# Performance work log

Measured on AMD Instinct MI355X. Metric: run time of the kernel, lower is better.

The kernel has to match this reference:

```python
import jax, jax.numpy as jnp
import numpy as np

B, S, DM, H, FF = 2, 2048, 1024, 16, 4096
DH = DM // H
EPS = 1e-5


def setup_inputs() -> dict:
    key = jax.random.key(0)
    ks = jax.random.split(key, 16)
    s = 0.02
    return {
        "x": jax.random.normal(ks[0], (B, S, DM), jnp.float32),
        "mask": jnp.ones((B, S), jnp.int32),
        "Wq": jax.random.normal(ks[1], (DM, DM), jnp.float32) * s,
        "bq": jnp.zeros((DM,), jnp.float32),
        "Wk": jax.random.normal(ks[2], (DM, DM), jnp.float32) * s,
        "bk": jnp.zeros((DM,), jnp.float32),
        "Wv": jax.random.normal(ks[3], (DM, DM), jnp.float32) * s,
        "bv": jnp.zeros((DM,), jnp.float32),
        "Wo": jax.random.normal(ks[4], (DM, DM), jnp.float32) * s,
        "bo": jnp.zeros((DM,), jnp.float32),
        "W1": jax.random.normal(ks[5], (DM, FF), jnp.float32) * s,
        "b1": jnp.zeros((FF,), jnp.float32),
        "W2": jax.random.normal(ks[6], (FF, DM), jnp.float32) * s,
        "b2": jnp.zeros((DM,), jnp.float32),
        "g1": jnp.ones((DM,), jnp.float32),
        "beta1": jnp.zeros((DM,), jnp.float32),
        "g2": jnp.ones((DM,), jnp.float32),
        "beta2": jnp.zeros((DM,), jnp.float32),
    }


def _layer_norm(x, g, b):
    mu = jnp.mean(x, axis=-1, keepdims=True)
    var = jnp.var(x, axis=-1, keepdims=True)
    return (x - mu) * jax.lax.rsqrt(var + EPS) * g + b


def reference(x, mask, Wq, bq, Wk, bk, Wv, bv, Wo, bo, W1, b1, W2, b2, g1, beta1, g2, beta2):
    # --- hollow multi-head attention ---
    q = (x @ Wq + bq).reshape(B, S, H, DH)
    k = (x @ Wk + bk).reshape(B, S, H, DH)
    v = (x @ Wv + bv).reshape(B, S, H, DH)
    scores = jnp.einsum("bqhd,bkhd->bhqk", q, k) / jnp.sqrt(jnp.float32(DH))
    # triu(diag=1) and tril(diag=-1) masks kill everything off-diagonal
    diag = jnp.eye(S, dtype=bool)  # [S, S]
    scores = jnp.where(diag[None, None], scores, -jnp.inf)
    attn = jax.nn.softmax(scores, axis=-1)
    out = jnp.einsum("bhqk,bkhd->bqhd", attn, v).reshape(B, S, DM)
    attn_out = out @ Wo + bo
    # --- residual + LN1 ---
    h = _layer_norm(x + attn_out, g1, beta1)
    # --- FFN ---
    ff = jax.nn.relu(h @ W1 + b1) @ W2 + b2
    # --- residual + LN2 ---
    return _layer_norm(h + ff, g2, beta2)
```

## Files before the change

### kernel.cpp

```cpp
#include <hip/hip_runtime.h>
#include <stdint.h>

typedef __bf16 bf16x8 __attribute__((ext_vector_type(8)));
typedef float f32x4 __attribute__((ext_vector_type(4)));

__device__ __forceinline__ uint16_t f2bf(float f) {
  union { float f; uint32_t u; } c; c.f = f;
  uint32_t u = c.u;
  u += 0x7fffu + ((u >> 16) & 1u);
  return (uint16_t)(u >> 16);
}
__device__ __forceinline__ float bf2f(uint16_t u) {
  union { uint32_t u; float f; } c; c.u = (uint32_t)u << 16; return c.f;
}

__device__ __forceinline__ void cvt_body(const float* __restrict__ in,
                                         uint16_t* __restrict__ out, int i) {
  float4 v = reinterpret_cast<const float4*>(in)[i];
  ushort4 o;
  o.x = f2bf(v.x); o.y = f2bf(v.y); o.z = f2bf(v.z); o.w = f2bf(v.w);
  reinterpret_cast<ushort4*>(out)[i] = o;
}

__global__ void prep_kernel(const float* __restrict__ x, const float* __restrict__ Wv,
                            const float* __restrict__ Wo, const float* __restrict__ W1,
                            const float* __restrict__ W2, const float* __restrict__ bv,
                            const float* __restrict__ bo,
                            uint16_t* __restrict__ xb, uint16_t* __restrict__ wvb,
                            uint16_t* __restrict__ woT, uint16_t* __restrict__ w1t,
                            uint16_t* __restrict__ w2t, float* __restrict__ bc) {
  __shared__ float tsh[32][33];
  __shared__ float red[8][32];
  int b = blockIdx.x;
  const int t = threadIdx.x;
  if (b < 4096) { cvt_body(x, xb, b * 256 + t); return; }
  b -= 4096;
  if (b < 1024) { cvt_body(Wv, wvb, b * 256 + t); return; }
  b -= 1024;

  const float* tin = nullptr; uint16_t* tout = nullptr;
  int R = 0, C = 0, bx = 0, by = 0;
  if (b < 1024) {
    tin = Wo; tout = woT; R = 1024; C = 1024; bx = b & 31; by = b >> 5;
  } else if (b < 1024 + 4096) {
    const int bb = b - 1024;
    tin = W1; tout = w1t; R = 1024; C = 4096; bx = bb & 127; by = bb >> 7;
  } else if (b < 1024 + 8192) {
    const int bb = b - (1024 + 4096);
    tin = W2; tout = w2t; R = 4096; C = 1024; bx = bb & 31; by = bb >> 5;
  } else {
    const int jb = b - (1024 + 8192);
    const int jl = t & 31, kg = t >> 5;
    const int j = jb * 32 + jl;
    float s = 0.f;
    const int k0 = kg * 128;
    for (int k = k0; k < k0 + 128; ++k) s += bv[k] * Wo[(size_t)k * 1024 + j];
    red[kg][jl] = s;
    __syncthreads();
    if (kg == 0) {
      float acc = bo[j];
#pragma unroll
      for (int q = 0; q < 8; ++q) acc += red[q][jl];
      bc[j] = acc;
    }
    return;
  }
  const int tx = t & 31, ty = t >> 5;
  const int c0 = bx * 32, r0 = by * 32;
#pragma unroll
  for (int i = 0; i < 4; ++i)
    tsh[ty + i * 8][tx] = tin[(size_t)(r0 + ty + i * 8) * C + (c0 + tx)];
  __syncthreads();
#pragma unroll
  for (int i = 0; i < 4; ++i)
    tout[(size_t)(c0 + ty + i * 8) * R + (r0 + tx)] = f2bf(tsh[tx][ty + i * 8]);
}

constexpr int BM = 128, BN = 128, BK = 64;

template <int MODE>
__launch_bounds__(256, 2)
__global__ void gemm2ph_kernel(const uint16_t* __restrict__ A, const uint16_t* __restrict__ Bt,
                               const float* __restrict__ bias, const float* __restrict__ res,
                               void* __restrict__ out, int M, int N, int Klen, int lda, int ldb) {
  __shared__ uint16_t sAB[2][2][BM * BK];
  const int tid  = threadIdx.x;
  const int lane = tid & 63;
  const int wave = tid >> 6;

  const int nwg = gridDim.x * gridDim.y;
  int wg = blockIdx.y * gridDim.x + blockIdx.x;
  wg = (wg & 7) * (nwg >> 3) + (wg >> 3);
  const int bx = wg % gridDim.x, by = wg / gridDim.x;
  const int m0 = by * BM, n0 = bx * BN;

  const int z = blockIdx.z;
  A  += (size_t)z * Klen;
  Bt += (size_t)z * Klen;

  const int wm = (wave >> 1) * 64;
  const int wn = (wave & 1) * 64;

  f32x4 acc[4][4] = {};

  const int srow = tid >> 3;
  const int scol = ((tid & 7) ^ (srow & 7)) * 8;
  const uint16_t* ga[4];
  const uint16_t* gb[4];
  uint32_t loff[4];
#pragma unroll
  for (int g = 0; g < 4; ++g) {
    const int row = srow + 32 * g;
    ga[g] = A + (size_t)(m0 + row) * lda + scol;
    gb[g] = Bt + (size_t)(n0 + row) * ldb + scol;
    loff[g] = (uint32_t)(tid + g * 256) * 8;
  }

  const int fr = lane & 15;
  const int hi = lane >> 4;
  const int rx = fr & 7;

  const int nk = Klen / BK;

#define STAGE2(buf, kt)                                                                   \
  {                                                                                       \
    _Pragma("unroll")                                                                     \
    for (int g = 0; g < 4; ++g) {                                                         \
      __builtin_amdgcn_global_load_lds(                                                   \
          (const __attribute__((address_space(1))) uint32_t*)(ga[g] + (size_t)(kt) * BK), \
          (__attribute__((address_space(3))) uint32_t*)(&sAB[buf][0][loff[g]]), 16, 0, 0);\
      __builtin_amdgcn_global_load_lds(                                                   \
          (const __attribute__((address_space(1))) uint32_t*)(gb[g] + (size_t)(kt) * BK), \
          (__attribute__((address_space(3))) uint32_t*)(&sAB[buf][1][loff[g]]), 16, 0, 0);\
    }                                                                                     \
  }

  STAGE2(0, 0);
  __syncthreads();

  int cur = 0;
  for (int kt = 0; kt < nk; ++kt) {
    if (kt + 1 < nk) STAGE2(cur ^ 1, kt + 1);
    const uint16_t* pA = &sAB[cur][0][0];
    const uint16_t* pB = &sAB[cur][1][0];
    bf16x8 af[4][2], bb[4][2];
#pragma unroll
    for (int m = 0; m < 4; ++m)
#pragma unroll
      for (int ks = 0; ks < 2; ++ks) {
        const int slot = (ks * 4 + hi) ^ rx;
        af[m][ks] = *reinterpret_cast<const bf16x8*>(pA + (wm + m * 16 + fr) * BK + slot * 8);
        bb[m][ks] = *reinterpret_cast<const bf16x8*>(pB + (wn + m * 16 + fr) * BK + slot * 8);
      }
#pragma unroll
    for (int ks = 0; ks < 2; ++ks)
#pragma unroll
      for (int m = 0; m < 4; ++m)
#pragma unroll
        for (int n = 0; n < 4; ++n)
          acc[m][n] = __builtin_amdgcn_mfma_f32_16x16x32_bf16(af[m][ks], bb[n][ks], acc[m][n], 0, 0, 0);
    __syncthreads();
    cur ^= 1;
  }
#undef STAGE2

  const int cn  = lane & 15;
  const int cm4 = (lane >> 4) * 4;
  uint16_t* outp = (uint16_t*)out + (size_t)z * M * N;
#pragma unroll
  for (int m = 0; m < 4; ++m) {
#pragma unroll
    for (int n = 0; n < 4; ++n) {
      const int gm = m0 + wm + m * 16 + cm4;
      const int gn = n0 + wn + n * 16 + cn;
      const float bbv = bias ? bias[gn] : 0.f;
#pragma unroll
      for (int r = 0; r < 4; ++r) {
        const size_t idx = (size_t)(gm + r) * N + gn;
        const float vv = acc[m][n][r] + bbv;
        if constexpr (MODE == 0) {
          outp[idx] = f2bf(vv);
        } else {
          ((uint16_t*)out)[idx] = f2bf(vv + res[idx]);
        }
      }
    }
  }
}

__global__ void comb4_kernel(const uint16_t* __restrict__ wp, size_t stride,
                             uint16_t* __restrict__ o, int n4) {
  const int i = blockIdx.x * 256 + threadIdx.x;
  if (i >= n4) return;
  float4 v = {0.f, 0.f, 0.f, 0.f};
#pragma unroll
  for (int zz = 0; zz < 4; ++zz) {
    const ushort4 p = reinterpret_cast<const ushort4*>(wp + zz * stride)[i];
    v.x += bf2f(p.x); v.y += bf2f(p.y); v.z += bf2f(p.z); v.w += bf2f(p.w);
  }
  ushort4 r;
  r.x = f2bf(v.x); r.y = f2bf(v.y); r.z = f2bf(v.z); r.w = f2bf(v.w);
  reinterpret_cast<ushort4*>(o)[i] = r;
}

template <int MODE>
__launch_bounds__(512, 2)
__global__ void gemm8ph_kernel(const uint16_t* __restrict__ A, const uint16_t* __restrict__ Bt,
                               const float* __restrict__ bias, void* __restrict__ out,
                               int M, int N, int Klen, int lda, int ldb) {
  extern __shared__ uint16_t lds[];
  const int tid  = threadIdx.x;
  const int lane = tid & 63;
  const int wave = tid >> 6;

  const int nwg = gridDim.x * gridDim.y;
  int wg = blockIdx.y * gridDim.x + blockIdx.x;
  wg = (wg & 7) * (nwg >> 3) + (wg >> 3);
  const int bx = wg % gridDim.x, by = wg / gridDim.x;
  const int m0 = by * 256, n0 = bx * 256;

  const int z = blockIdx.z;
  A  += (size_t)z * Klen;
  Bt += (size_t)z * Klen;

  const int wm = (wave >> 2) * 128;
  const int wn = (wave & 3) * 64;

  f32x4 acc[8][4] = {};

  const int srw = tid >> 3;
  const int sp  = tid & 7;
  const uint16_t* gu[8];
#pragma unroll
  for (int u = 0; u < 8; ++u) {
    const uint16_t* base = (u < 4) ? A + (size_t)(m0 + u * 64) * lda
                                   : Bt + (size_t)(n0 + (u - 4) * 64) * ldb;
    const int ld = (u < 4) ? lda : ldb;
    gu[u] = base + (size_t)srw * ld + ((sp ^ (srw & 7)) * 8);
  }

  const int nk = Klen / 64;

#define STAGE8(T, U)                                                                          \
  if ((T) < nk) {                                                                             \
    __builtin_amdgcn_global_load_lds(                                                         \
        (const __attribute__((address_space(1))) uint32_t*)(gu[U] + (size_t)(T) * 64),        \
        (__attribute__((address_space(3))) uint32_t*)(lds + ((T) & 1) * 32768 + (U) * 4096 +  \
                                                      tid * 8),                               \
        16, 0, 0);                                                                            \
  }

  const int fr = lane & 15;
  const int hi = lane >> 4;
  int aoff[8];
#pragma unroll
  for (int m = 0; m < 8; ++m) {
    const int u = (wm >> 6) + (m >> 2);
    const int R = (m & 3) * 16 + fr;
    aoff[m] = u * 4096 + R * 64 + ((hi ^ (R & 7)) * 8);
  }
  int boff[4];
#pragma unroll
  for (int n = 0; n < 4; ++n) {
    const int u = 4 + (wn >> 6);
    const int R = n * 16 + fr;
    boff[n] = u * 4096 + R * 64 + ((hi ^ (R & 7)) * 8);
  }

  STAGE8(0, 0); STAGE8(0, 1); STAGE8(0, 2); STAGE8(0, 3);
  STAGE8(0, 4); STAGE8(0, 5); STAGE8(0, 6); STAGE8(0, 7);
  STAGE8(1, 4); STAGE8(1, 5); STAGE8(1, 6); STAGE8(1, 7);
  asm volatile("s_waitcnt vmcnt(4)" ::: "memory");
  __builtin_amdgcn_s_barrier();

#define LD8(off) (*reinterpret_cast<const bf16x8*>(bufp + (off)))
#define PHASE_MFMA32(KS)                                                      \
  __builtin_amdgcn_s_setprio(1);                                              \
  _Pragma("unroll") for (int mm = 0; mm < 8; ++mm)                            \
    _Pragma("unroll") for (int n = 0; n < 4; ++n)                             \
      acc[mm][n] = __builtin_amdgcn_mfma_f32_16x16x32_bf16(                   \
          aq[mm], bq[n][KS], acc[mm][n], 0, 0, 0);                            \
  __builtin_amdgcn_s_setprio(0);

  for (int k = 0; k < nk; ++k) {
    const uint16_t* bufp = lds + (k & 1) * 32768;
    bf16x8 bq[4][2], aq[8];
#pragma unroll
    for (int n = 0; n < 4; ++n) { bq[n][0] = LD8(boff[n]); bq[n][1] = LD8(boff[n] ^ 32); }
#pragma unroll
    for (int mm = 0; mm < 8; ++mm) aq[mm] = LD8(aoff[mm]);
    STAGE8(k + 1, 0); STAGE8(k + 1, 1); STAGE8(k + 1, 2); STAGE8(k + 1, 3);
    PHASE_MFMA32(0);
    asm volatile("s_waitcnt lgkmcnt(0)" ::: "memory");
    __builtin_amdgcn_s_barrier();
#pragma unroll
    for (int mm = 0; mm < 8; ++mm) aq[mm] = LD8(aoff[mm] ^ 32);
    STAGE8(k + 2, 4); STAGE8(k + 2, 5); STAGE8(k + 2, 6); STAGE8(k + 2, 7);
    PHASE_MFMA32(1);
    if (k < nk - 2) { asm volatile("s_waitcnt vmcnt(4)" ::: "memory"); }
    else            { asm volatile("s_waitcnt vmcnt(0)" ::: "memory"); }
    asm volatile("s_waitcnt lgkmcnt(0)" ::: "memory");
    __builtin_amdgcn_s_barrier();
  }
#undef PHASE_MFMA32
#undef LD8
#undef STAGE8

  const int cn  = lane & 15;
  const int cm4 = (lane >> 4) * 4;
  uint16_t* outp = (uint16_t*)out;
  if constexpr (MODE == 1) outp += (size_t)z * M * N;
  float bias_n[4];
  if constexpr (MODE == 0) {
#pragma unroll
    for (int n = 0; n < 4; ++n) bias_n[n] = bias[n0 + wn + n * 16 + cn];
  }
#pragma unroll
  for (int m = 0; m < 8; ++m) {
#pragma unroll
    for (int n = 0; n < 4; ++n) {
      const int gm = m0 + wm + m * 16 + cm4;
      const int gn = n0 + wn + n * 16 + cn;
#pragma unroll
      for (int r = 0; r < 4; ++r) {
        const size_t idx = (size_t)(gm + r) * N + gn;
        if constexpr (MODE == 0) {
          outp[idx] = f2bf(fmaxf(acc[m][n][r] + bias_n[n], 0.f));
        } else {
          outp[idx] = f2bf(acc[m][n][r]);
        }
      }
    }
  }
}

__global__ void ln1_kernel(const uint16_t* __restrict__ q0, const uint16_t* __restrict__ q1,
                           const uint16_t* __restrict__ xb, const float* __restrict__ bc,
                           const float* __restrict__ g, const float* __restrict__ b,
                           uint16_t* __restrict__ outb) {
  const int row = blockIdx.x;
  const int t = threadIdx.x;
  const size_t base = (size_t)row * 1024;
  const ushort4 a4 = reinterpret_cast<const ushort4*>(q0 + base)[t];
  const ushort4 b4 = reinterpret_cast<const ushort4*>(q1 + base)[t];
  const ushort4 x4 = reinterpret_cast<const ushort4*>(xb + base)[t];
  const float4 c4 = reinterpret_cast<const float4*>(bc)[t];
  float4 v;
  v.x = bf2f(a4.x) + bf2f(b4.x) + bf2f(x4.x) + c4.x;
  v.y = bf2f(a4.y) + bf2f(b4.y) + bf2f(x4.y) + c4.y;
  v.z = bf2f(a4.z) + bf2f(b4.z) + bf2f(x4.z) + c4.z;
  v.w = bf2f(a4.w) + bf2f(b4.w) + bf2f(x4.w) + c4.w;
  float s  = v.x + v.y + v.z + v.w;
  float s2 = v.x * v.x + v.y * v.y + v.z * v.z + v.w * v.w;
#pragma unroll
  for (int o = 32; o > 0; o >>= 1) { s += __shfl_down(s, o); s2 += __shfl_down(s2, o); }
  __shared__ float red[8];
  const int lane = t & 63, wave = t >> 6;
  if (lane == 0) { red[wave] = s; red[4 + wave] = s2; }
  __syncthreads();
  const float S  = red[0] + red[1] + red[2] + red[3];
  const float S2 = red[4] + red[5] + red[6] + red[7];
  const float mu  = S * (1.f / 1024.f);
  const float var = S2 * (1.f / 1024.f) - mu * mu;
  const float rs  = rsqrtf(var + 1e-5f);
  const float4 gg = reinterpret_cast<const float4*>(g)[t];
  const float4 bb = reinterpret_cast<const float4*>(b)[t];
  ushort4 ob;
  ob.x = f2bf((v.x - mu) * rs * gg.x + bb.x);
  ob.y = f2bf((v.y - mu) * rs * gg.y + bb.y);
  ob.z = f2bf((v.z - mu) * rs * gg.z + bb.z);
  ob.w = f2bf((v.w - mu) * rs * gg.w + bb.w);
  reinterpret_cast<ushort4*>(outb + base)[t] = ob;
}

__global__ void ln2_kernel(const uint16_t* __restrict__ pp, size_t pstride,
                           const uint16_t* __restrict__ hb, const float* __restrict__ b2,
                           const float* __restrict__ g, const float* __restrict__ be,
                           float* __restrict__ out) {
  const int row = blockIdx.x;
  const int t = threadIdx.x;
  const size_t base = (size_t)row * 1024;
  const ushort4 h4 = reinterpret_cast<const ushort4*>(hb + base)[t];
  const float4 c2 = reinterpret_cast<const float4*>(b2)[t];
  float4 v;
  v.x = c2.x + bf2f(h4.x); v.y = c2.y + bf2f(h4.y);
  v.z = c2.z + bf2f(h4.z); v.w = c2.w + bf2f(h4.w);
#pragma unroll
  for (int zz = 0; zz < 4; ++zz) {
    const ushort4 p4 = reinterpret_cast<const ushort4*>(pp + zz * pstride + base)[t];
    v.x += bf2f(p4.x); v.y += bf2f(p4.y); v.z += bf2f(p4.z); v.w += bf2f(p4.w);
  }
  float s  = v.x + v.y + v.z + v.w;
  float s2 = v.x * v.x + v.y * v.y + v.z * v.z + v.w * v.w;
#pragma unroll
  for (int o = 32; o > 0; o >>= 1) { s += __shfl_down(s, o); s2 += __shfl_down(s2, o); }
  __shared__ float red[8];
  const int lane = t & 63, wave = t >> 6;
  if (lane == 0) { red[wave] = s; red[4 + wave] = s2; }
  __syncthreads();
  const float S  = red[0] + red[1] + red[2] + red[3];
  const float S2 = red[4] + red[5] + red[6] + red[7];
  const float mu  = S * (1.f / 1024.f);
  const float var = S2 * (1.f / 1024.f) - mu * mu;
  const float rs  = rsqrtf(var + 1e-5f);
  const float4 gg = reinterpret_cast<const float4*>(g)[t];
  const float4 bb = reinterpret_cast<const float4*>(be)[t];
  float4 o;
  o.x = (v.x - mu) * rs * gg.x + bb.x;
  o.y = (v.y - mu) * rs * gg.y + bb.y;
  o.z = (v.z - mu) * rs * gg.z + bb.z;
  o.w = (v.w - mu) * rs * gg.w + bb.w;
  reinterpret_cast<float4*>(out + base)[t] = o;
}

extern "C" void kernel_launch(void* const* d_in, const int* in_sizes, int n_in,
                              void* d_out, int out_size, void* d_ws, size_t ws_size,
                              hipStream_t stream) {
  const float* x   = (const float*)d_in[0];
  const float* Wv  = (const float*)d_in[6];
  const float* bv  = (const float*)d_in[7];
  const float* Wo  = (const float*)d_in[8];
  const float* bo  = (const float*)d_in[9];
  const float* W1  = (const float*)d_in[10];
  const float* b1  = (const float*)d_in[11];
  const float* W2  = (const float*)d_in[12];
  const float* b2  = (const float*)d_in[13];
  const float* g1  = (const float*)d_in[14];
  const float* be1 = (const float*)d_in[15];
  const float* g2  = (const float*)d_in[16];
  const float* be2 = (const float*)d_in[17];
  float* out = (float*)d_out;

  constexpr int M = 4096, DM = 1024, FF = 4096;

  char* p = (char*)d_ws;
  auto alloc = [&](size_t bytes) {
    char* r = p;
    p += (bytes + 255) & ~(size_t)255;
    return r;
  };
  uint16_t* xb  = (uint16_t*)alloc((size_t)M * DM * 2);
  uint16_t* wvb = (uint16_t*)alloc((size_t)DM * DM * 2);
  uint16_t* woT = (uint16_t*)alloc((size_t)DM * DM * 2);
  uint16_t* w1t = (uint16_t*)alloc((size_t)FF * DM * 2);
  uint16_t* w2t = (uint16_t*)alloc((size_t)DM * FF * 2);
  uint16_t* wcT = (uint16_t*)alloc((size_t)DM * DM * 2);
  float*    bc  = (float*)   alloc((size_t)DM * 4);
  uint16_t* hb  = (uint16_t*)alloc((size_t)M * DM * 2);
  uint16_t* tb  = (uint16_t*)alloc((size_t)M * FF * 2);
  uint16_t* pp  = (uint16_t*)alloc((size_t)4 * M * DM * 2);
  uint16_t* wp = pp;
  uint16_t* q  = tb;

  (void)hipFuncSetAttribute(reinterpret_cast<const void*>(gemm8ph_kernel<0>),
                            hipFuncAttributeMaxDynamicSharedMemorySize, 131072);
  (void)hipFuncSetAttribute(reinterpret_cast<const void*>(gemm8ph_kernel<1>),
                            hipFuncAttributeMaxDynamicSharedMemorySize, 131072);

  prep_kernel<<<4096 + 1024 + 1024 + 4096 + 4096 + 32, 256, 0, stream>>>(
      x, Wv, Wo, W1, W2, bv, bo, xb, wvb, woT, w1t, w2t, bc);

  gemm2ph_kernel<0><<<dim3(DM / BN, DM / BM, 4), 256, 0, stream>>>(
      woT, wvb, nullptr, nullptr, wp, DM, DM, DM / 4, DM, DM);
  comb4_kernel<<<DM * DM / 4 / 256, 256, 0, stream>>>(wp, (size_t)DM * DM, wcT, DM * DM / 4);
  gemm2ph_kernel<0><<<dim3(DM / BN, M / BM, 2), 256, 0, stream>>>(
      xb, wcT, nullptr, nullptr, q, M, DM, DM / 2, DM, DM);
  ln1_kernel<<<M, 256, 0, stream>>>(q, q + (size_t)M * DM, xb, bc, g1, be1, hb);
  gemm8ph_kernel<0><<<dim3(FF / 256, M / 256), 512, 131072, stream>>>(
      hb, w1t, b1, tb, M, FF, DM, DM, DM);
  gemm8ph_kernel<1><<<dim3(DM / 256, M / 256, 4), 512, 131072, stream>>>(
      tb, w2t, nullptr, pp, M, DM, FF / 4, FF, FF);
  ln2_kernel<<<M, 256, 0, stream>>>(pp, (size_t)M * DM, hb, b2, g2, be2, out);
}
```

Measured before the change: 138.8 us.

## Split A/B LDS staging with triple-buffered B and single barrier per k-step

```diff
diff --git a/kernel.cpp b/kernel.cpp
--- a/kernel.cpp
+++ b/kernel.cpp
@@ -241,13 +241,25 @@
 
   const int nk = Klen / 64;
 
-#define STAGE8(T, U)                                                                          \
+#define STAGE_A(T)                                                                            \
   if ((T) < nk) {                                                                             \
-    __builtin_amdgcn_global_load_lds(                                                         \
-        (const __attribute__((address_space(1))) uint32_t*)(gu[U] + (size_t)(T) * 64),        \
-        (__attribute__((address_space(3))) uint32_t*)(lds + ((T) & 1) * 32768 + (U) * 4096 +  \
-                                                      tid * 8),                               \
-        16, 0, 0);                                                                            \
+    _Pragma("unroll")                                                                         \
+    for (int u = 0; u < 4; ++u)                                                               \
+      __builtin_amdgcn_global_load_lds(                                                       \
+          (const __attribute__((address_space(1))) uint32_t*)(gu[u] + (size_t)(T) * 64),      \
+          (__attribute__((address_space(3))) uint32_t*)(lds + ((T) & 1) * 16384 + u * 4096 +  \
+                                                        tid * 8),                             \
+          16, 0, 0);                                                                          \
+  }
+#define STAGE_B(T, BUF)                                                                       \
+  if ((T) < nk) {                                                                             \
+    _Pragma("unroll")                                                                         \
+    for (int u = 4; u < 8; ++u)                                                               \
+      __builtin_amdgcn_global_load_lds(                                                       \
+          (const __attribute__((address_space(1))) uint32_t*)(gu[u] + (size_t)(T) * 64),      \
+          (__attribute__((address_space(3))) uint32_t*)(lds + 32768 + (BUF) * 16384 +         \
+                                                        (u - 4) * 4096 + tid * 8),            \
+          16, 0, 0);                                                                          \
   }
 
   const int fr = lane & 15;
@@ -262,49 +274,50 @@
   int boff[4];
 #pragma unroll
   for (int n = 0; n < 4; ++n) {
-    const int u = 4 + (wn >> 6);
+    const int u = wn >> 6;
     const int R = n * 16 + fr;
     boff[n] = u * 4096 + R * 64 + ((hi ^ (R & 7)) * 8);
   }
 
-  STAGE8(0, 0); STAGE8(0, 1); STAGE8(0, 2); STAGE8(0, 3);
-  STAGE8(0, 4); STAGE8(0, 5); STAGE8(0, 6); STAGE8(0, 7);
-  STAGE8(1, 4); STAGE8(1, 5); STAGE8(1, 6); STAGE8(1, 7);
+  STAGE_A(0);
+  STAGE_B(0, 0);
+  STAGE_B(1, 1);
   asm volatile("s_waitcnt vmcnt(4)" ::: "memory");
   __builtin_amdgcn_s_barrier();
 
-#define LD8(off) (*reinterpret_cast<const bf16x8*>(bufp + (off)))
-#define PHASE_MFMA32(KS)                                                      \
+#define LD8(p, off) (*reinterpret_cast<const bf16x8*>((p) + (off)))
+#define MFMA32(AQ, KS)                                                        \
   __builtin_amdgcn_s_setprio(1);                                              \
   _Pragma("unroll") for (int mm = 0; mm < 8; ++mm)                            \
     _Pragma("unroll") for (int n = 0; n < 4; ++n)                             \
       acc[mm][n] = __builtin_amdgcn_mfma_f32_16x16x32_bf16(                   \
-          aq[mm], bq[n][KS], acc[mm][n], 0, 0, 0);                            \
+          AQ[mm], bq[n][KS], acc[mm][n], 0, 0, 0);                            \
   __builtin_amdgcn_s_setprio(0);
 
+  int bcur = 0, b2 = 2;
   for (int k = 0; k < nk; ++k) {
-    const uint16_t* bufp = lds + (k & 1) * 32768;
-    bf16x8 bq[4][2], aq[8];
-#pragma unroll
-    for (int n = 0; n < 4; ++n) { bq[n][0] = LD8(boff[n]); bq[n][1] = LD8(boff[n] ^ 32); }
-#pragma unroll
-    for (int mm = 0; mm < 8; ++mm) aq[mm] = LD8(aoff[mm]);
-    STAGE8(k + 1, 0); STAGE8(k + 1, 1); STAGE8(k + 1, 2); STAGE8(k + 1, 3);
-    PHASE_MFMA32(0);
-    asm volatile("s_waitcnt lgkmcnt(0)" ::: "memory");
-    __builtin_amdgcn_s_barrier();
-#pragma unroll
-    for (int mm = 0; mm < 8; ++mm) aq[mm] = LD8(aoff[mm] ^ 32);
-    STAGE8(k + 2, 4); STAGE8(k + 2, 5); STAGE8(k + 2, 6); STAGE8(k + 2, 7);
-    PHASE_MFMA32(1);
+    const uint16_t* bufA = lds + (k & 1) * 16384;
+    const uint16_t* bufB = lds + 32768 + bcur * 16384;
+    bf16x8 bq[4][2], aq0[8], aq1[8];
+#pragma unroll
+    for (int n = 0; n < 4; ++n) { bq[n][0] = LD8(bufB, boff[n]); bq[n][1] = LD8(bufB, boff[n] ^ 32); }
+#pragma unroll
+    for (int mm = 0; mm < 8; ++mm) { aq0[mm] = LD8(bufA, aoff[mm]); aq1[mm] = LD8(bufA, aoff[mm] ^ 32); }
+    STAGE_A(k + 1);
+    STAGE_B(k + 2, b2);
+    MFMA32(aq0, 0);
+    MFMA32(aq1, 1);
     if (k < nk - 2) { asm volatile("s_waitcnt vmcnt(4)" ::: "memory"); }
     else            { asm volatile("s_waitcnt vmcnt(0)" ::: "memory"); }
     asm volatile("s_waitcnt lgkmcnt(0)" ::: "memory");
     __builtin_amdgcn_s_barrier();
-  }
-#undef PHASE_MFMA32
+    bcur = (bcur == 2) ? 0 : bcur + 1;
+    b2   = (b2 == 2)   ? 0 : b2 + 1;
+  }
+#undef MFMA32
 #undef LD8
-#undef STAGE8
+#undef STAGE_A
+#undef STAGE_B
 
   const int cn  = lane & 15;
   const int cm4 = (lane >> 4) * 4;
@@ -453,9 +466,9 @@
   uint16_t* q  = tb;
 
   (void)hipFuncSetAttribute(reinterpret_cast<const void*>(gemm8ph_kernel<0>),
-                            hipFuncAttributeMaxDynamicSharedMemorySize, 131072);
+                            hipFuncAttributeMaxDynamicSharedMemorySize, 163840);
   (void)hipFuncSetAttribute(reinterpret_cast<const void*>(gemm8ph_kernel<1>),
-                            hipFuncAttributeMaxDynamicSharedMemorySize, 131072);
+                            hipFuncAttributeMaxDynamicSharedMemorySize, 163840);
 
   prep_kernel<<<4096 + 1024 + 1024 + 4096 + 4096 + 32, 256, 0, stream>>>(
       x, Wv, Wo, W1, W2, bv, bo, xb, wvb, woT, w1t, w2t, bc);
@@ -466,9 +479,9 @@
   gemm2ph_kernel<0><<<dim3(DM / BN, M / BM, 2), 256, 0, stream>>>(
       xb, wcT, nullptr, nullptr, q, M, DM, DM / 2, DM, DM);
   ln1_kernel<<<M, 256, 0, stream>>>(q, q + (size_t)M * DM, xb, bc, g1, be1, hb);
-  gemm8ph_kernel<0><<<dim3(FF / 256, M / 256), 512, 131072, stream>>>(
+  gemm8ph_kernel<0><<<dim3(FF / 256, M / 256), 512, 163840, stream>>>(
       hb, w1t, b1, tb, M, FF, DM, DM, DM);
-  gemm8ph_kernel<1><<<dim3(DM / 256, M / 256, 4), 512, 131072, stream>>>(
+  gemm8ph_kernel<1><<<dim3(DM / 256, M / 256, 4), 512, 163840, stream>>>(
       tb, w2t, nullptr, pp, M, DM, FF / 4, FF, FF);
   ln2_kernel<<<M, 256, 0, stream>>>(pp, (size_t)M * DM, hb, b2, g2, be2, out);
 }
```

After: 152.4 us. 1.1x slower.
